# Kernel optimization log

Measured on AMD Instinct MI355X. Metric: run time of the kernel, lower is better.

Reference implementation:

```python
import jax, jax.numpy as jnp
import numpy as np

N_FILTERS = 40
FILTER_SIZE = 401   # int(16000*25/1000), forced odd
POOL_STRIDE = 160   # int(16000*10/1000)
EPS = 1e-6
S_SMOOTH = 0.04     # fixed PCEN smoothing coefficient s
DELTA = 2.0         # fixed PCEN bias delta
R_MIN, R_MAX = 0.2, 1.0
HIDDEN = 32


def setup_inputs() -> dict:
    key = jax.random.key(0)
    ks = jax.random.split(key, 6)
    B, L = 8, 160000
    x = jax.random.normal(ks[0], (B, L), dtype=jnp.float32)
    # mel-initialized Gabor params (as in mel_filter_params)
    sr, fmin, fmax = 16000.0, 60.0, 7800.0
    min_mel = 1127.0 * np.log1p(fmin / 700.0)
    max_mel = 1127.0 * np.log1p(fmax / 700.0)
    peaks_mel = np.linspace(min_mel, max_mel, N_FILTERS + 2)
    peaks_hz = 700.0 * np.expm1(peaks_mel / 1127.0)
    center_freqs = jnp.asarray(peaks_hz[1:-1] * 2.0 * np.pi / sr, dtype=jnp.float32)
    z = np.sqrt(2.0 * np.log(2.0)) / np.pi
    bandwidths = jnp.asarray(z * sr / (peaks_hz[2:] - peaks_hz[:-2]), dtype=jnp.float32)
    pooling_widths = jnp.full((N_FILTERS,), 0.4, dtype=jnp.float32)
    # GRU (input_size=1, hidden=32) + head Linear(32,32)->ReLU->Linear(32,2)
    def gl(k, shape):
        return jax.random.normal(k, shape, dtype=jnp.float32) * 0.1
    w_ih = gl(ks[1], (3 * HIDDEN, 1))
    w_hh = gl(ks[2], (3 * HIDDEN, HIDDEN))
    b_ih = jnp.zeros((3 * HIDDEN,), jnp.float32)
    b_hh = jnp.zeros((3 * HIDDEN,), jnp.float32)
    hw1 = gl(ks[3], (32, HIDDEN)); hb1 = jnp.zeros((32,), jnp.float32)
    hw2 = gl(ks[4], (2, 32)); hb2 = jnp.zeros((2,), jnp.float32)
    return dict(x=x, center_freqs=center_freqs, bandwidths=bandwidths,
                pooling_widths=pooling_widths, w_ih=w_ih, w_hh=w_hh,
                b_ih=b_ih, b_hh=b_hh, hw1=hw1, hb1=hb1, hw2=hw2, hb2=hb2)


def _gabor_filterbank(x, center_freqs, bandwidths, pooling_widths):
    z = np.sqrt(2.0 * np.log(2.0)) / np.pi
    cf = jnp.clip(center_freqs, 0.0, np.pi)
    bw = jnp.clip(bandwidths, 4.0 * z, FILTER_SIZE * z)
    t = jnp.arange(-(FILTER_SIZE // 2), (FILTER_SIZE + 1) // 2, dtype=jnp.float32)
    denom = 1.0 / (jnp.sqrt(2.0 * np.pi) * bw)                        # [F]
    gauss = jnp.exp(-(t[None, :] ** 2) / (2.0 * bw[:, None] ** 2))    # [F,K]
    phase = cf[:, None] * t[None, :]                                  # [F,K]
    fr = denom[:, None] * gauss * jnp.cos(phase)
    fi = denom[:, None] * gauss * jnp.sin(phase)
    filt = jnp.concatenate([fr, fi], axis=0)[:, None, :]              # [2F,1,K]
    pad = FILTER_SIZE // 2
    y = jax.lax.conv_general_dilated(x[:, None, :], filt, (1,), [(pad, pad)])
    y = y ** 2
    y = y[:, :N_FILTERS] + y[:, N_FILTERS:]                           # squared modulus [B,F,L]
    pw = jnp.clip(pooling_widths, 2.0 / FILTER_SIZE, 0.5)
    tt = jnp.arange(FILTER_SIZE, dtype=jnp.float32) / (FILTER_SIZE - 1) - 0.5
    win = jnp.exp(-0.5 * (tt[None, :] / pw[:, None]) ** 2)[:, None, :]  # [F,1,K]
    y = jax.lax.conv_general_dilated(y, win, (POOL_STRIDE,), [(pad, pad)],
                                     feature_group_count=N_FILTERS)
    return y  # [B,F,T]


def _gru_cell(h, xin, w_ih, w_hh, b_ih, b_hh):
    gi = xin @ w_ih.T + b_ih   # [N,3H]
    gh = h @ w_hh.T + b_hh
    i_r, i_z, i_n = jnp.split(gi, 3, axis=-1)
    h_r, h_z, h_n = jnp.split(gh, 3, axis=-1)
    r = jax.nn.sigmoid(i_r + h_r)
    zz = jax.nn.sigmoid(i_z + h_z)
    n = jnp.tanh(i_n + r * h_n)
    return (1.0 - zz) * n + zz * h


def _adaptive_pcen(frames, w_ih, w_hh, b_ih, b_hh, hw1, hb1, hw2, hb2):
    B, F, T = frames.shape
    Xt = jnp.transpose(frames, (2, 0, 1))  # [T,B,F]

    def controller(x_prev, x_t):  # each [B,F] -> per-bin (alpha, r)
        xp = x_prev.reshape(-1, 1)
        xc = x_t.reshape(-1, 1)
        h = jnp.zeros((B * F, HIDDEN), frames.dtype)
        h = _gru_cell(h, xp, w_ih, w_hh, b_ih, b_hh)
        h = _gru_cell(h, xc, w_ih, w_hh, b_ih, b_hh)
        hid = jax.nn.relu(h @ hw1.T + hb1)
        logits = hid @ hw2.T + hb2  # [B*F,2]
        alpha = jax.nn.sigmoid(logits[:, 0]).reshape(B, F)
        r = (R_MIN + (R_MAX - R_MIN) * jax.nn.sigmoid(logits[:, 1])).reshape(B, F)
        return alpha, r

    def step(carry, X_t):
        M_prev, X_prev = carry
        alpha, r = controller(X_prev, X_t)
        M_t = (1.0 - S_SMOOTH) * M_prev + S_SMOOTH * X_t
        out = (X_t / (M_t + EPS) ** alpha + DELTA) ** r - DELTA ** r
        return (M_t, X_t), out

    init = (jnp.zeros((B, F), frames.dtype), Xt[0])
    _, outs = jax.lax.scan(step, init, Xt)
    return jnp.transpose(outs, (1, 2, 0))  # [B,F,T]


def reference(x, center_freqs, bandwidths, pooling_widths,
              w_ih, w_hh, b_ih, b_hh, hw1, hb1, hw2, hb2):
    frames = _gabor_filterbank(x, center_freqs, bandwidths, pooling_widths)
    return _adaptive_pcen(frames, w_ih, w_hh, b_ih, b_hh, hw1, hb1, hw2, hb2)
```

## Files before the change

kernel.cpp:

```cpp
#include <hip/hip_runtime.h>
#include <math.h>

#define NF 40
#define FS 401
#define AST 424
#define PSTRIDE 160
#define BB 8
#define LL 160000
#define PADL 256
#define LST 161024
#define TOUT 1000
#define NTILE 512
#define NCHUNKC 313
#define ROWCH 121
#define ROWST (ROWCH*8)
#define EROW 520
#define TCP 32
#define NCHUNKP 32
#define PELEM (TCP*PSTRIDE + 408)
#define WROW 402
#define NCONVB 5032

typedef __attribute__((ext_vector_type(8))) _Float16 half8v;
typedef __attribute__((ext_vector_type(4))) _Float16 half4v;
typedef __attribute__((ext_vector_type(2))) _Float16 half2v;
typedef __attribute__((ext_vector_type(4))) float float4v;
typedef _Float16 f16;

__device__ __forceinline__ float sigm(float x) { return 1.0f / (1.0f + __expf(-x)); }
__device__ __forceinline__ float tanh_fast(float x) { return 1.0f - 2.0f / (__expf(2.0f * x) + 1.0f); }

__global__ __launch_bounds__(256) void prep_all(
    const float* __restrict__ x, const float* __restrict__ cf_,
    const float* __restrict__ bw_, const float* __restrict__ pw_,
    f16* __restrict__ xb, f16* __restrict__ Ag, float* __restrict__ winG)
{
    int blk = blockIdx.x;
    if (blk < NCONVB) {
        int i = blk * 256 + threadIdx.x;
        int b = i / LST, o = i % LST;
        float v = 0.0f;
        if (o >= PADL && o < PADL + LL) v = x[b * LL + (o - PADL)];
        xb[i] = (f16)v;
        return;
    }
    const float PI_F = 3.14159265358979323846f;
    if (blk < NCONVB + 80) {
        int row = blk - NCONVB;
        int f = row >> 1, comp = row & 1;
        float Z = sqrtf(2.0f * logf(2.0f)) / PI_F;
        float cf = fminf(fmaxf(cf_[f], 0.0f), PI_F);
        float bw = fminf(fmaxf(bw_[f], 4.0f * Z), 401.0f * Z);
        float denom = 1.0f / (sqrtf(2.0f * PI_F) * bw);
        float inv2 = 1.0f / (2.0f * bw * bw);
        for (int k = threadIdx.x; k < AST; k += 256) {
            float v = 0.0f;
            if (k < FS) {
                float t = (float)(k - 200);
                float g = denom * expf(-(t * t) * inv2);
                float sv, cv;
                sincosf(cf * t, &sv, &cv);
                v = comp ? g * sv : g * cv;
            }
            Ag[row * AST + k] = (f16)v;
        }
        return;
    }
    int f = blk - NCONVB - 80;
    float pw = fminf(fmaxf(pw_[f], 2.0f / 401.0f), 0.5f);
    float invpw = 1.0f / pw;
    for (int j = threadIdx.x; j < WROW; j += 256) {
        float w = 0.0f;
        if (j < FS) {
            float tt = (float)j * (1.0f / 400.0f) - 0.5f;
            float u = tt * invpw;
            w = expf(-0.5f * u * u);
        }
        winG[f * WROW + j] = w;
    }
}

__global__ __launch_bounds__(256, 2) void conv_mfma(
    const f16* __restrict__ xb,
    const f16* __restrict__ Ag,
    f16* __restrict__ eb)
{
    __shared__ __align__(16) unsigned char smem[40 * EROW * 2];
    f16* slab = (f16*)smem;
    f16* eL   = (f16*)smem;

    int chunk = blockIdx.x;
    int bi = blockIdx.y;
    int p0 = chunk * NTILE;
    int pbase = PADL + p0 - 200;
    const f16* xs = xb + (size_t)bi * LST;
    int tid = threadIdx.x;

    for (int sc = tid; sc < 8 * 120; sc += 256) {
        int r = sc / 120, m = sc - r * 120;
        int s0 = pbase + 8 * m + (r & ~1);
        const uint* gp = (const uint*)(xs + s0);
        uint v0 = gp[0], v1 = gp[1], v2 = gp[2], v3 = gp[3], v4 = gp[4];
        if (r & 1) {
            v0 = __builtin_amdgcn_alignbyte(v1, v0, 2);
            v1 = __builtin_amdgcn_alignbyte(v2, v1, 2);
            v2 = __builtin_amdgcn_alignbyte(v3, v2, 2);
            v3 = __builtin_amdgcn_alignbyte(v4, v3, 2);
        }
        *(uint4*)(&slab[r * ROWST + 8 * m]) = make_uint4(v0, v1, v2, v3);
    }
    __syncthreads();

    int wv = tid >> 6, lane = tid & 63, q = lane >> 4, l15 = lane & 15;

    float4v acc[5][8];
#pragma unroll
    for (int t = 0; t < 5; ++t)
#pragma unroll
        for (int s = 0; s < 8; ++s)
            acc[t][s] = (float4v){0.f, 0.f, 0.f, 0.f};

    const f16* aP[5];
    const f16* bPtr[10];
#pragma unroll
    for (int t = 0; t < 5; ++t) aP[t] = Ag + (16 * t + l15) * AST + 8 * q;
#pragma unroll
    for (int s = 0; s < 10; ++s) {
        int pos = 128 * wv + 16 * s + l15;
        bPtr[s] = slab + (pos & 7) * ROWST + 8 * ((pos >> 3) + q);
    }

    half8v bf[8];
#pragma unroll
    for (int s = 0; s < 8; ++s) bf[s] = *(const half8v*)(bPtr[s]);

#pragma unroll
    for (int kk = 0; kk < 13; ++kk) {
        int k = 32 * kk;
        half8v af[5];
#pragma unroll
        for (int t = 0; t < 5; ++t) af[t] = *(const half8v*)(aP[t] + k);
        half8v nb0, nb1;
        if (kk < 12) {
            nb0 = *(const half8v*)(bPtr[8] + k);
            nb1 = *(const half8v*)(bPtr[9] + k);
        }
#pragma unroll
        for (int t = 0; t < 5; ++t)
#pragma unroll
            for (int s = 0; s < 8; ++s)
                acc[t][s] = __builtin_amdgcn_mfma_f32_16x16x32_f16(af[t], bf[s], acc[t][s], 0, 0, 0);
        if (kk < 12) {
#pragma unroll
            for (int s = 0; s < 6; ++s) bf[s] = bf[s + 2];
            bf[6] = nb0; bf[7] = nb1;
        }
    }

    __syncthreads();

#pragma unroll
    for (int t = 0; t < 5; ++t) {
        int f0 = 8 * t + 2 * q;
#pragma unroll
        for (int s = 0; s < 8; ++s) {
            float4v a = acc[t][s];
            int pl = 128 * wv + 16 * s + l15;
            eL[f0 * EROW + pl] = (f16)(a.x * a.x + a.y * a.y);
            eL[(f0 + 1) * EROW + pl] = (f16)(a.z * a.z + a.w * a.w);
        }
    }
    __syncthreads();

    f16* ebb = eb + (size_t)bi * NF * LL;
#pragma unroll
    for (int it = 0; it < 10; ++it) {
        int idx = it * 256 + tid;
        int row = idx >> 6;
        int off = (idx & 63) * 8;
        if (p0 + off < LL) {
            uint4 v = *(const uint4*)(&eL[row * EROW + off]);
            *(uint4*)(&ebb[row * LL + p0 + off]) = v;
        }
    }
}

__global__ __launch_bounds__(256) void pool_kernel(
    const f16* __restrict__ eb, const float* __restrict__ winG, float* __restrict__ Xout)
{
    __shared__ __align__(16) f16 es[PELEM + 8];
    __shared__ __align__(16) float win[416];
    int chunk = blockIdx.x;
    int f = blockIdx.y;
    int bi = blockIdx.z;
    int tau0 = chunk * TCP;
    int start = tau0 * PSTRIDE - 200;
    int tid = threadIdx.x;

    for (int k = tid; k < 416; k += 256)
        win[k] = (k < WROW) ? winG[f * WROW + k] : 0.0f;

    const f16* erow = eb + ((size_t)bi * NF + f) * LL;
    if (start >= 0 && start + PELEM <= LL) {
        for (int j = tid; j < PELEM / 8; j += 256)
            *(uint4*)(&es[8 * j]) = *(const uint4*)(erow + start + 8 * j);
    } else {
        for (int j = tid; j < PELEM; j += 256) {
            int p = start + j;
            es[j] = (p >= 0 && p < LL) ? erow[p] : (f16)0.0f;
        }
    }
    __syncthreads();

    int ft = tid >> 4, l16 = tid & 15;
#pragma unroll
    for (int pass = 0; pass < 2; ++pass) {
        int frame = pass * 16 + ft;
        int base = frame * PSTRIDE;
        float acc = 0.0f;
#pragma unroll
        for (int m = 0; m < 13; ++m) {
            int kw = 2 * l16 + 32 * m;
            half2v ep = *(const half2v*)(&es[base + kw]);
            float2 wp = *(const float2*)(&win[kw]);
            acc = fmaf((float)ep[0], wp.x, acc);
            acc = fmaf((float)ep[1], wp.y, acc);
        }
#pragma unroll
        for (int off = 8; off > 0; off >>= 1)
            acc += __shfl_down(acc, off, 16);
        int tau = tau0 + frame;
        if (l16 == 0 && tau < TOUT)
            Xout[((size_t)bi * NF + f) * TOUT + tau] = acc;
    }
}

__global__ __launch_bounds__(256) void pcen_scan_kernel(
    const float* __restrict__ X, float* __restrict__ M)
{
    int wid = (blockIdx.x * 256 + threadIdx.x) >> 6;
    int lane = threadIdx.x & 63;
    if (wid >= BB * NF) return;
    const float a1 = 0.96f;
    const float a2 = a1 * a1;
    const float a4 = a2 * a2;
    const float a8 = a4 * a4;
    const float a16 = a8 * a8;
    const float a32 = a16 * a16;
    const float ss = 0.04f;
    float al1 = powf(a1, (float)(lane + 1));
    float carry = 0.0f;
    const float* row = X + wid * TOUT;
    float* mrow = M + wid * TOUT;

    for (int c = 0; c < TOUT; c += 64) {
        int t = c + lane;
        float v = (t < TOUT) ? row[t] : 0.0f;
        float y = ss * v;
        float u;
        u = __shfl_up(y, 1, 64);  if (lane >= 1)  y = fmaf(a1, u, y);
        u = __shfl_up(y, 2, 64);  if (lane >= 2)  y = fmaf(a2, u, y);
        u = __shfl_up(y, 4, 64);  if (lane >= 4)  y = fmaf(a4, u, y);
        u = __shfl_up(y, 8, 64);  if (lane >= 8)  y = fmaf(a8, u, y);
        u = __shfl_up(y, 16, 64); if (lane >= 16) y = fmaf(a16, u, y);
        u = __shfl_up(y, 32, 64); if (lane >= 32) y = fmaf(a32, u, y);
        y = fmaf(al1, carry, y);
        carry = __shfl(y, 63, 64);
        if (t < TOUT) mrow[t] = y;
    }
}

__global__ __launch_bounds__(256) void pcen_ctrl_mfma(
    const float* __restrict__ X, const float* __restrict__ M,
    const float* __restrict__ w_ih, const float* __restrict__ w_hh,
    const float* __restrict__ b_ih, const float* __restrict__ b_hh,
    const float* __restrict__ hw1, const float* __restrict__ hb1,
    const float* __restrict__ hw2, const float* __restrict__ hb2,
    float* __restrict__ out)
{
    __shared__ f16 s_whhA[96 * 40];
    __shared__ f16 s_w1A[32 * 40];
    __shared__ __align__(16) float4 s_A1[32];
    __shared__ __align__(16) float4 s_A2[32];
    __shared__ float s_hb1[32];
    __shared__ float s_hw2[64];
    __shared__ float s_hb2[2];
    __shared__ f16 sh1[4][16 * 40];
    __shared__ f16 sh2[4][16 * 40];

    int tid = threadIdx.x;
    for (int i = tid; i < 96 * 32; i += 256) {
        int m = i >> 5, k = i & 31;
        s_whhA[m * 40 + k] = (f16)w_hh[i];
    }
    for (int i = tid; i < 32 * 32; i += 256) {
        int m = i >> 5, k = i & 31;
        s_w1A[m * 40 + k] = (f16)hw1[i];
    }
    if (tid < 32) {
        int j = tid;
        s_A1[j] = make_float4(w_ih[j], b_ih[j] + b_hh[j],
                              w_ih[32 + j], b_ih[32 + j] + b_hh[32 + j]);
        s_A2[j] = make_float4(w_ih[64 + j], b_ih[64 + j], b_hh[64 + j], 0.0f);
        s_hb1[j] = hb1[j];
    }
    if (tid < 64) s_hw2[tid] = hw2[tid];
    if (tid < 2)  s_hb2[tid] = hb2[tid];
    __syncthreads();

    int wv = tid >> 6, lane = tid & 63;
    int c = lane & 15, q = lane >> 4;
    int waveBase = blockIdx.x * 256 + wv * 64;

#pragma unroll
    for (int g = 0; g < 4; ++g) {
        int idx0 = waveBase + g * 16;
        int idxc = idx0 + c;
        int tt0 = idx0 % TOUT + c;
        float xc = X[idxc];
        float xp = (tt0 == 0 || tt0 == TOUT) ? xc : X[idxc - 1];
        float mv = M[idxc];

        float h1v[8];
#pragma unroll
        for (int jj = 0; jj < 8; ++jj) {
            int j = (jj < 4) ? (4 * q + jj) : (16 + 4 * q + (jj - 4));
            float4 a1 = s_A1[j];
            float4 a2 = s_A2[j];
            float r = sigm(fmaf(xp, a1.x, a1.y));
            float z = sigm(fmaf(xp, a1.z, a1.w));
            float n = tanh_fast(fmaf(xp, a2.x, a2.y) + r * a2.z);
            h1v[jj] = (1.0f - z) * n;
        }

        {
            half4v lo = {(f16)h1v[0], (f16)h1v[1], (f16)h1v[2], (f16)h1v[3]};
            half4v hi = {(f16)h1v[4], (f16)h1v[5], (f16)h1v[6], (f16)h1v[7]};
            *(half4v*)(&sh1[wv][c * 40 + 4 * q]) = lo;
            *(half4v*)(&sh1[wv][c * 40 + 16 + 4 * q]) = hi;
        }

        float4v acc[6];
        {
            half8v bfv = *(const half8v*)(&sh1[wv][c * 40 + 8 * q]);
#pragma unroll
            for (int t = 0; t < 6; ++t) {
                half8v af = *(const half8v*)(&s_whhA[(16 * t + c) * 40 + 8 * q]);
                acc[t] = __builtin_amdgcn_mfma_f32_16x16x32_f16(af, bfv, (float4v){0.f,0.f,0.f,0.f}, 0, 0, 0);
            }
        }

        float h2v[8];
#pragma unroll
        for (int jj = 0; jj < 8; ++jj) {
            int j = (jj < 4) ? (4 * q + jj) : (16 + 4 * q + (jj - 4));
            int reg = jj & 3;
            float accR = (jj < 4) ? acc[0][reg] : acc[1][reg];
            float accZ = (jj < 4) ? acc[2][reg] : acc[3][reg];
            float accN = (jj < 4) ? acc[4][reg] : acc[5][reg];
            float4 a1 = s_A1[j];
            float4 a2 = s_A2[j];
            float r = sigm(fmaf(xc, a1.x, a1.y) + accR);
            float z = sigm(fmaf(xc, a1.z, a1.w) + accZ);
            float gn = accN + a2.z;
            float n = tanh_fast(fmaf(xc, a2.x, a2.y) + r * gn);
            h2v[jj] = fmaf(z, h1v[jj] - n, n);
        }

        {
            half4v lo = {(f16)h2v[0], (f16)h2v[1], (f16)h2v[2], (f16)h2v[3]};
            half4v hi = {(f16)h2v[4], (f16)h2v[5], (f16)h2v[6], (f16)h2v[7]};
            *(half4v*)(&sh2[wv][c * 40 + 4 * q]) = lo;
            *(half4v*)(&sh2[wv][c * 40 + 16 + 4 * q]) = hi;
        }

        float4v hacc[2];
        {
            half8v bfv = *(const half8v*)(&sh2[wv][c * 40 + 8 * q]);
#pragma unroll
            for (int t = 0; t < 2; ++t) {
                half8v af = *(const half8v*)(&s_w1A[(16 * t + c) * 40 + 8 * q]);
                hacc[t] = __builtin_amdgcn_mfma_f32_16x16x32_f16(af, bfv, (float4v){0.f,0.f,0.f,0.f}, 0, 0, 0);
            }
        }

        float p0 = 0.f, p1 = 0.f;
#pragma unroll
        for (int jj = 0; jj < 8; ++jj) {
            int i = (jj < 4) ? (4 * q + jj) : (16 + 4 * q + (jj - 4));
            int reg = jj & 3;
            float hv = (jj < 4) ? hacc[0][reg] : hacc[1][reg];
            hv = fmaxf(hv + s_hb1[i], 0.0f);
            p0 = fmaf(hv, s_hw2[i], p0);
            p1 = fmaf(hv, s_hw2[32 + i], p1);
        }
        p0 += __shfl_xor(p0, 16);
        p0 += __shfl_xor(p0, 32);
        p1 += __shfl_xor(p1, 16);
        p1 += __shfl_xor(p1, 32);

        float alpha = sigm(p0 + s_hb2[0]);
        float rr = fmaf(0.8f, sigm(p1 + s_hb2[1]), 0.2f);
        float md = __expf(alpha * __logf(mv + 1e-6f));
        float bse = xc / md + 2.0f;
        float val = __expf(rr * __logf(bse)) - __expf(rr * 0.69314718056f);
        if (q == 0)
            out[idxc] = val;
    }
}

extern "C" void kernel_launch(void* const* d_in, const int* in_sizes, int n_in,
                              void* d_out, int out_size, void* d_ws, size_t ws_size,
                              hipStream_t stream) {
    const float* x    = (const float*)d_in[0];
    const float* cf   = (const float*)d_in[1];
    const float* bw   = (const float*)d_in[2];
    const float* pw   = (const float*)d_in[3];
    const float* w_ih = (const float*)d_in[4];
    const float* w_hh = (const float*)d_in[5];
    const float* b_ih = (const float*)d_in[6];
    const float* b_hh = (const float*)d_in[7];
    const float* hw1  = (const float*)d_in[8];
    const float* hb1  = (const float*)d_in[9];
    const float* hw2  = (const float*)d_in[10];
    const float* hb2  = (const float*)d_in[11];
    float* out = (float*)d_out;

    const size_t xb_b = (size_t)BB * LST * 2;
    const size_t ag_b = (size_t)80 * AST * 2;
    const size_t wg_b = (size_t)NF * WROW * 4;
    const size_t xm_b = (size_t)2 * BB * NF * TOUT * 4;
    size_t fixed = xb_b + ag_b + wg_b + xm_b;
    size_t e_per_batch = (size_t)NF * LL * 2;
    int nb;
    if (ws_size >= fixed + 8 * e_per_batch)      nb = 8;
    else if (ws_size >= fixed + 2 * e_per_batch) nb = 2;
    else                                         nb = 1;
    int nslice = BB / nb;

    f16* xb    = (f16*)d_ws;
    f16* Ag    = xb + (size_t)BB * LST;
    float* winG = (float*)(Ag + (size_t)80 * AST);
    f16* ebuf  = (f16*)(winG + (size_t)NF * WROW);
    float* Xf  = (float*)(ebuf + (size_t)nb * NF * LL);
    float* Mf  = Xf + (size_t)BB * NF * TOUT;

    prep_all<<<dim3(NCONVB + 80 + NF), dim3(256), 0, stream>>>(x, cf, bw, pw, xb, Ag, winG);

    for (int sl = 0; sl < nslice; ++sl) {
        conv_mfma<<<dim3(NCHUNKC, nb), dim3(256), 0, stream>>>(
            xb + (size_t)sl * nb * LST, Ag, ebuf);
        pool_kernel<<<dim3(NCHUNKP, NF, nb), dim3(256), 0, stream>>>(
            ebuf, winG, Xf + (size_t)sl * nb * NF * TOUT);
    }

    pcen_scan_kernel<<<dim3((BB * NF * 64) / 256), dim3(256), 0, stream>>>(Xf, Mf);
    pcen_ctrl_mfma<<<dim3((BB * NF * TOUT) / 256), dim3(256), 0, stream>>>(
        Xf, Mf, w_ih, w_hh, b_ih, b_hh, hw1, hb1, hw2, hb2, out);
}
```

Measured before the change: 265.9 us.

## Fuse pooling, PCEN scan and controller into one per-row tail kernel

Replaces the pool, scan and controller kernels with a single 1024-thread block per (batch, filter) row. The block pools the row in eight shared-memory chunks, runs the smoothing scan in shared memory, then evaluates the GRU controller and PCEN output. This removes two launches and the global round trips for the X and M intermediates. In exchange the tail runs on only 40×nb blocks with a serial chunk loop and a single-wave scan, so GPU occupancy and parallelism drop sharply.

```diff
diff --git a/kernel.cpp b/kernel.cpp
--- a/kernel.cpp
+++ b/kernel.cpp
@@ -15,11 +15,10 @@
 #define ROWCH 121
 #define ROWST (ROWCH*8)
 #define EROW 520
-#define TCP 32
-#define NCHUNKP 32
-#define PELEM (TCP*PSTRIDE + 408)
 #define WROW 402
 #define NCONVB 5032
+#define TAUC 125
+#define ECH (TAUC*PSTRIDE + 408)
 
 typedef __attribute__((ext_vector_type(8))) _Float16 half8v;
 typedef __attribute__((ext_vector_type(4))) _Float16 half4v;
@@ -185,99 +184,18 @@
     }
 }
 
-__global__ __launch_bounds__(256) void pool_kernel(
-    const f16* __restrict__ eb, const float* __restrict__ winG, float* __restrict__ Xout)
-{
-    __shared__ __align__(16) f16 es[PELEM + 8];
-    __shared__ __align__(16) float win[416];
-    int chunk = blockIdx.x;
-    int f = blockIdx.y;
-    int bi = blockIdx.z;
-    int tau0 = chunk * TCP;
-    int start = tau0 * PSTRIDE - 200;
-    int tid = threadIdx.x;
-
-    for (int k = tid; k < 416; k += 256)
-        win[k] = (k < WROW) ? winG[f * WROW + k] : 0.0f;
-
-    const f16* erow = eb + ((size_t)bi * NF + f) * LL;
-    if (start >= 0 && start + PELEM <= LL) {
-        for (int j = tid; j < PELEM / 8; j += 256)
-            *(uint4*)(&es[8 * j]) = *(const uint4*)(erow + start + 8 * j);
-    } else {
-        for (int j = tid; j < PELEM; j += 256) {
-            int p = start + j;
-            es[j] = (p >= 0 && p < LL) ? erow[p] : (f16)0.0f;
-        }
-    }
-    __syncthreads();
-
-    int ft = tid >> 4, l16 = tid & 15;
-#pragma unroll
-    for (int pass = 0; pass < 2; ++pass) {
-        int frame = pass * 16 + ft;
-        int base = frame * PSTRIDE;
-        float acc = 0.0f;
-#pragma unroll
-        for (int m = 0; m < 13; ++m) {
-            int kw = 2 * l16 + 32 * m;
-            half2v ep = *(const half2v*)(&es[base + kw]);
-            float2 wp = *(const float2*)(&win[kw]);
-            acc = fmaf((float)ep[0], wp.x, acc);
-            acc = fmaf((float)ep[1], wp.y, acc);
-        }
-#pragma unroll
-        for (int off = 8; off > 0; off >>= 1)
-            acc += __shfl_down(acc, off, 16);
-        int tau = tau0 + frame;
-        if (l16 == 0 && tau < TOUT)
-            Xout[((size_t)bi * NF + f) * TOUT + tau] = acc;
-    }
-}
-
-__global__ __launch_bounds__(256) void pcen_scan_kernel(
-    const float* __restrict__ X, float* __restrict__ M)
-{
-    int wid = (blockIdx.x * 256 + threadIdx.x) >> 6;
-    int lane = threadIdx.x & 63;
-    if (wid >= BB * NF) return;
-    const float a1 = 0.96f;
-    const float a2 = a1 * a1;
-    const float a4 = a2 * a2;
-    const float a8 = a4 * a4;
-    const float a16 = a8 * a8;
-    const float a32 = a16 * a16;
-    const float ss = 0.04f;
-    float al1 = powf(a1, (float)(lane + 1));
-    float carry = 0.0f;
-    const float* row = X + wid * TOUT;
-    float* mrow = M + wid * TOUT;
-
-    for (int c = 0; c < TOUT; c += 64) {
-        int t = c + lane;
-        float v = (t < TOUT) ? row[t] : 0.0f;
-        float y = ss * v;
-        float u;
-        u = __shfl_up(y, 1, 64);  if (lane >= 1)  y = fmaf(a1, u, y);
-        u = __shfl_up(y, 2, 64);  if (lane >= 2)  y = fmaf(a2, u, y);
-        u = __shfl_up(y, 4, 64);  if (lane >= 4)  y = fmaf(a4, u, y);
-        u = __shfl_up(y, 8, 64);  if (lane >= 8)  y = fmaf(a8, u, y);
-        u = __shfl_up(y, 16, 64); if (lane >= 16) y = fmaf(a16, u, y);
-        u = __shfl_up(y, 32, 64); if (lane >= 32) y = fmaf(a32, u, y);
-        y = fmaf(al1, carry, y);
-        carry = __shfl(y, 63, 64);
-        if (t < TOUT) mrow[t] = y;
-    }
-}
-
-__global__ __launch_bounds__(256) void pcen_ctrl_mfma(
-    const float* __restrict__ X, const float* __restrict__ M,
+__global__ __launch_bounds__(1024, 4) void tail_kernel(
+    const f16* __restrict__ eb,
+    const float* __restrict__ winG,
     const float* __restrict__ w_ih, const float* __restrict__ w_hh,
     const float* __restrict__ b_ih, const float* __restrict__ b_hh,
     const float* __restrict__ hw1, const float* __restrict__ hb1,
     const float* __restrict__ hw2, const float* __restrict__ hb2,
     float* __restrict__ out)
 {
+    __shared__ __align__(16) float win[416];
+    __shared__ __align__(16) float xs[1024];
+    __shared__ __align__(16) float ms[1024];
     __shared__ f16 s_whhA[96 * 40];
     __shared__ f16 s_w1A[32 * 40];
     __shared__ __align__(16) float4 s_A1[32];
@@ -285,15 +203,18 @@
     __shared__ float s_hb1[32];
     __shared__ float s_hw2[64];
     __shared__ float s_hb2[2];
-    __shared__ f16 sh1[4][16 * 40];
-    __shared__ f16 sh2[4][16 * 40];
-
+    __shared__ __align__(16) unsigned char ureg[41024];
+    f16* es = (f16*)ureg;
+
+    int f = blockIdx.x;
+    int bi = blockIdx.y;
     int tid = threadIdx.x;
-    for (int i = tid; i < 96 * 32; i += 256) {
+
+    for (int i = tid; i < 96 * 32; i += 1024) {
         int m = i >> 5, k = i & 31;
         s_whhA[m * 40 + k] = (f16)w_hh[i];
     }
-    for (int i = tid; i < 32 * 32; i += 256) {
+    for (int i = tid; i < 32 * 32; i += 1024) {
         int m = i >> 5, k = i & 31;
         s_w1A[m * 40 + k] = (f16)hw1[i];
     }
@@ -306,20 +227,83 @@
     }
     if (tid < 64) s_hw2[tid] = hw2[tid];
     if (tid < 2)  s_hb2[tid] = hb2[tid];
+    if (tid < 416) win[tid] = (tid < WROW) ? winG[f * WROW + tid] : 0.0f;
+    if (tid >= 1000) { xs[tid] = 0.0f; ms[tid] = 0.0f; }
     __syncthreads();
 
+    const f16* erow = eb + ((size_t)bi * NF + f) * LL;
+    int ft = tid >> 4, l16 = tid & 15;
+    for (int c = 0; c < 8; ++c) {
+        int start = c * (TAUC * PSTRIDE) - 200;
+        if (c > 0 && c < 7) {
+            for (int j = tid; j < ECH / 8; j += 1024)
+                *(uint4*)(&es[8 * j]) = *(const uint4*)(erow + start + 8 * j);
+        } else {
+            for (int j = tid; j < ECH; j += 1024) {
+                int p = start + j;
+                es[j] = (p >= 0 && p < LL) ? erow[p] : (f16)0.0f;
+            }
+        }
+        __syncthreads();
+#pragma unroll
+        for (int pass = 0; pass < 2; ++pass) {
+            int tauL = pass * 64 + ft;
+            if (tauL < TAUC) {
+                int base = tauL * PSTRIDE;
+                float acc = 0.0f;
+#pragma unroll
+                for (int m = 0; m < 13; ++m) {
+                    int kw = 2 * l16 + 32 * m;
+                    half2v ep = *(const half2v*)(&es[base + kw]);
+                    float2 wp = *(const float2*)(&win[kw]);
+                    acc = fmaf((float)ep[0], wp.x, acc);
+                    acc = fmaf((float)ep[1], wp.y, acc);
+                }
+#pragma unroll
+                for (int off = 8; off > 0; off >>= 1)
+                    acc += __shfl_down(acc, off, 16);
+                if (l16 == 0) xs[c * TAUC + tauL] = acc;
+            }
+        }
+        __syncthreads();
+    }
+
+    if (tid < 64) {
+        int lane = tid;
+        const float a1 = 0.96f;
+        const float a2 = a1 * a1, a4 = a2 * a2, a8 = a4 * a4;
+        const float a16 = a8 * a8, a32 = a16 * a16;
+        float al1 = powf(a1, (float)(lane + 1));
+        float carry = 0.0f;
+        for (int c = 0; c < TOUT; c += 64) {
+            float y = 0.04f * xs[c + lane];
+            float u;
+            u = __shfl_up(y, 1, 64);  if (lane >= 1)  y = fmaf(a1, u, y);
+            u = __shfl_up(y, 2, 64);  if (lane >= 2)  y = fmaf(a2, u, y);
+            u = __shfl_up(y, 4, 64);  if (lane >= 4)  y = fmaf(a4, u, y);
+            u = __shfl_up(y, 8, 64);  if (lane >= 8)  y = fmaf(a8, u, y);
+            u = __shfl_up(y, 16, 64); if (lane >= 16) y = fmaf(a16, u, y);
+            u = __shfl_up(y, 32, 64); if (lane >= 32) y = fmaf(a32, u, y);
+            y = fmaf(al1, carry, y);
+            carry = __shfl(y, 63, 64);
+            ms[c + lane] = y;
+        }
+    }
+    __syncthreads();
+
     int wv = tid >> 6, lane = tid & 63;
-    int c = lane & 15, q = lane >> 4;
-    int waveBase = blockIdx.x * 256 + wv * 64;
+    int c16 = lane & 15, q = lane >> 4;
+    f16* sh1 = (f16*)(ureg + wv * 2560);
+    f16* sh2 = (f16*)(ureg + wv * 2560 + 1280);
+    float* outb = out + ((size_t)bi * NF + f) * TOUT;
 
 #pragma unroll
     for (int g = 0; g < 4; ++g) {
-        int idx0 = waveBase + g * 16;
-        int idxc = idx0 + c;
-        int tt0 = idx0 % TOUT + c;
-        float xc = X[idxc];
-        float xp = (tt0 == 0 || tt0 == TOUT) ? xc : X[idxc - 1];
-        float mv = M[idxc];
+        int t = (wv * 4 + g) * 16 + c16;
+        int tc = (t < TOUT) ? t : (TOUT - 1);
+        float xc = xs[tc];
+        float xp = (tc == 0) ? xc : xs[tc - 1];
+        float mv = ms[tc];
 
         float h1v[8];
 #pragma unroll
@@ -332,24 +316,21 @@
             float n = tanh_fast(fmaf(xp, a2.x, a2.y) + r * a2.z);
             h1v[jj] = (1.0f - z) * n;
         }
-
         {
             half4v lo = {(f16)h1v[0], (f16)h1v[1], (f16)h1v[2], (f16)h1v[3]};
             half4v hi = {(f16)h1v[4], (f16)h1v[5], (f16)h1v[6], (f16)h1v[7]};
-            *(half4v*)(&sh1[wv][c * 40 + 4 * q]) = lo;
-            *(half4v*)(&sh1[wv][c * 40 + 16 + 4 * q]) = hi;
-        }
-
+            *(half4v*)(&sh1[c16 * 40 + 4 * q]) = lo;
+            *(half4v*)(&sh1[c16 * 40 + 16 + 4 * q]) = hi;
+        }
         float4v acc[6];
         {
-            half8v bfv = *(const half8v*)(&sh1[wv][c * 40 + 8 * q]);
-#pragma unroll
-            for (int t = 0; t < 6; ++t) {
-                half8v af = *(const half8v*)(&s_whhA[(16 * t + c) * 40 + 8 * q]);
-                acc[t] = __builtin_amdgcn_mfma_f32_16x16x32_f16(af, bfv, (float4v){0.f,0.f,0.f,0.f}, 0, 0, 0);
+            half8v bfv = *(const half8v*)(&sh1[c16 * 40 + 8 * q]);
+#pragma unroll
+            for (int tt = 0; tt < 6; ++tt) {
+                half8v af = *(const half8v*)(&s_whhA[(16 * tt + c16) * 40 + 8 * q]);
+                acc[tt] = __builtin_amdgcn_mfma_f32_16x16x32_f16(af, bfv, (float4v){0.f,0.f,0.f,0.f}, 0, 0, 0);
             }
         }
-
         float h2v[8];
 #pragma unroll
         for (int jj = 0; jj < 8; ++jj) {
@@ -366,24 +347,21 @@
             float n = tanh_fast(fmaf(xc, a2.x, a2.y) + r * gn);
             h2v[jj] = fmaf(z, h1v[jj] - n, n);
         }
-
         {
             half4v lo = {(f16)h2v[0], (f16)h2v[1], (f16)h2v[2], (f16)h2v[3]};
             half4v hi = {(f16)h2v[4], (f16)h2v[5], (f16)h2v[6], (f16)h2v[7]};
-            *(half4v*)(&sh2[wv][c * 40 + 4 * q]) = lo;
-            *(half4v*)(&sh2[wv][c * 40 + 16 + 4 * q]) = hi;
-        }
-
+            *(half4v*)(&sh2[c16 * 40 + 4 * q]) = lo;
+            *(half4v*)(&sh2[c16 * 40 + 16 + 4 * q]) = hi;
+        }
         float4v hacc[2];
         {
-            half8v bfv = *(const half8v*)(&sh2[wv][c * 40 + 8 * q]);
-#pragma unroll
-            for (int t = 0; t < 2; ++t) {
-                half8v af = *(const half8v*)(&s_w1A[(16 * t + c) * 40 + 8 * q]);
-                hacc[t] = __builtin_amdgcn_mfma_f32_16x16x32_f16(af, bfv, (float4v){0.f,0.f,0.f,0.f}, 0, 0, 0);
+            half8v bfv = *(const half8v*)(&sh2[c16 * 40 + 8 * q]);
+#pragma unroll
+            for (int tt = 0; tt < 2; ++tt) {
+                half8v af = *(const half8v*)(&s_w1A[(16 * tt + c16) * 40 + 8 * q]);
+                hacc[tt] = __builtin_amdgcn_mfma_f32_16x16x32_f16(af, bfv, (float4v){0.f,0.f,0.f,0.f}, 0, 0, 0);
             }
         }
-
         float p0 = 0.f, p1 = 0.f;
 #pragma unroll
         for (int jj = 0; jj < 8; ++jj) {
@@ -404,8 +382,8 @@
         float md = __expf(alpha * __logf(mv + 1e-6f));
         float bse = xc / md + 2.0f;
         float val = __expf(rr * __logf(bse)) - __expf(rr * 0.69314718056f);
-        if (q == 0)
-            out[idxc] = val;
+        if (q == 0 && t < TOUT)
+            outb[t] = val;
     }
 }
 
@@ -429,8 +407,7 @@
     const size_t xb_b = (size_t)BB * LST * 2;
     const size_t ag_b = (size_t)80 * AST * 2;
     const size_t wg_b = (size_t)NF * WROW * 4;
-    const size_t xm_b = (size_t)2 * BB * NF * TOUT * 4;
-    size_t fixed = xb_b + ag_b + wg_b + xm_b;
+    size_t fixed = xb_b + ag_b + wg_b;
     size_t e_per_batch = (size_t)NF * LL * 2;
     int nb;
     if (ws_size >= fixed + 8 * e_per_batch)      nb = 8;
@@ -438,23 +415,18 @@
     else                                         nb = 1;
     int nslice = BB / nb;
 
-    f16* xb    = (f16*)d_ws;
-    f16* Ag    = xb + (size_t)BB * LST;
+    f16* xb     = (f16*)d_ws;
+    f16* Ag     = xb + (size_t)BB * LST;
     float* winG = (float*)(Ag + (size_t)80 * AST);
-    f16* ebuf  = (f16*)(winG + (size_t)NF * WROW);
-    float* Xf  = (float*)(ebuf + (size_t)nb * NF * LL);
-    float* Mf  = Xf + (size_t)BB * NF * TOUT;
+    f16* ebuf   = (f16*)(winG + (size_t)NF * WROW);
 
     prep_all<<<dim3(NCONVB + 80 + NF), dim3(256), 0, stream>>>(x, cf, bw, pw, xb, Ag, winG);
 
     for (int sl = 0; sl < nslice; ++sl) {
         conv_mfma<<<dim3(NCHUNKC, nb), dim3(256), 0, stream>>>(
             xb + (size_t)sl * nb * LST, Ag, ebuf);
-        pool_kernel<<<dim3(NCHUNKP, NF, nb), dim3(256), 0, stream>>>(
-            ebuf, winG, Xf + (size_t)sl * nb * NF * TOUT);
-    }
-
-    pcen_scan_kernel<<<dim3((BB * NF * 64) / 256), dim3(256), 0, stream>>>(Xf, Mf);
-    pcen_ctrl_mfma<<<dim3((BB * NF * TOUT) / 256), dim3(256), 0, stream>>>(
-        Xf, Mf, w_ih, w_hh, b_ih, b_hh, hw1, hb1, hw2, hb2, out);
+        tail_kernel<<<dim3(NF, nb), dim3(1024), 0, stream>>>(
+            ebuf, winG, w_ih, w_hh, b_ih, b_hh, hw1, hb1, hw2, hb2,
+            out + (size_t)sl * nb * NF * TOUT);
+    }
 }
```

New measurement: 299.6 us. +12.7%, slower.

## Shrink conv LDS staging via two-pass epilogue; spread PCEN controller over more blocks

Applied to the files above, without the earlier changes.

The conv epilogue now writes the squared-magnitude tile to LDS in two passes (16 filters, then 24), so the shared buffer shrinks from 40 rows to 24. That lowers LDS use per block and may allow more resident blocks, at the cost of extra barriers. The PCEN controller kernel now has each wave handle 16 outputs instead of looping over 64, launching four times as many blocks to raise parallelism. The cost is repeated per-block weight staging into LDS.

```diff
diff --git a/kernel.cpp b/kernel.cpp
--- a/kernel.cpp
+++ b/kernel.cpp
@@ -15,10 +15,10 @@
 #define ROWCH 121
 #define ROWST (ROWCH*8)
 #define EROW 520
+#define WROW 402
 #define TCP 32
 #define NCHUNKP 32
 #define PELEM (TCP*PSTRIDE + 408)
-#define WROW 402
 #define NCONVB 5032
 
 typedef __attribute__((ext_vector_type(8))) _Float16 half8v;
@@ -85,7 +85,7 @@
     const f16* __restrict__ Ag,
     f16* __restrict__ eb)
 {
-    __shared__ __align__(16) unsigned char smem[40 * EROW * 2];
+    __shared__ __align__(16) unsigned char smem[24 * EROW * 2];
     f16* slab = (f16*)smem;
     f16* eL   = (f16*)smem;
 
@@ -159,8 +159,10 @@
 
     __syncthreads();
 
-#pragma unroll
-    for (int t = 0; t < 5; ++t) {
+    f16* ebb = eb + (size_t)bi * NF * LL;
+
+#pragma unroll
+    for (int t = 0; t < 2; ++t) {
         int f0 = 8 * t + 2 * q;
 #pragma unroll
         for (int s = 0; s < 8; ++s) {
@@ -171,16 +173,38 @@
         }
     }
     __syncthreads();
-
-    f16* ebb = eb + (size_t)bi * NF * LL;
-#pragma unroll
-    for (int it = 0; it < 10; ++it) {
+#pragma unroll
+    for (int it = 0; it < 4; ++it) {
         int idx = it * 256 + tid;
         int row = idx >> 6;
         int off = (idx & 63) * 8;
         if (p0 + off < LL) {
             uint4 v = *(const uint4*)(&eL[row * EROW + off]);
             *(uint4*)(&ebb[row * LL + p0 + off]) = v;
+        }
+    }
+    __syncthreads();
+
+#pragma unroll
+    for (int t = 2; t < 5; ++t) {
+        int f0 = 8 * t + 2 * q;
+#pragma unroll
+        for (int s = 0; s < 8; ++s) {
+            float4v a = acc[t][s];
+            int pl = 128 * wv + 16 * s + l15;
+            eL[(f0 - 16) * EROW + pl] = (f16)(a.x * a.x + a.y * a.y);
+            eL[(f0 - 15) * EROW + pl] = (f16)(a.z * a.z + a.w * a.w);
+        }
+    }
+    __syncthreads();
+#pragma unroll
+    for (int it = 0; it < 6; ++it) {
+        int idx = it * 256 + tid;
+        int row = idx >> 6;
+        int off = (idx & 63) * 8;
+        if (p0 + off < LL) {
+            uint4 v = *(const uint4*)(&eL[row * EROW + off]);
+            *(uint4*)(&ebb[(row + 16) * LL + p0 + off]) = v;
         }
     }
 }
@@ -310,103 +334,99 @@
 
     int wv = tid >> 6, lane = tid & 63;
     int c = lane & 15, q = lane >> 4;
-    int waveBase = blockIdx.x * 256 + wv * 64;
-
-#pragma unroll
-    for (int g = 0; g < 4; ++g) {
-        int idx0 = waveBase + g * 16;
-        int idxc = idx0 + c;
-        int tt0 = idx0 % TOUT + c;
-        float xc = X[idxc];
-        float xp = (tt0 == 0 || tt0 == TOUT) ? xc : X[idxc - 1];
-        float mv = M[idxc];
-
-        float h1v[8];
-#pragma unroll
-        for (int jj = 0; jj < 8; ++jj) {
-            int j = (jj < 4) ? (4 * q + jj) : (16 + 4 * q + (jj - 4));
-            float4 a1 = s_A1[j];
-            float4 a2 = s_A2[j];
-            float r = sigm(fmaf(xp, a1.x, a1.y));
-            float z = sigm(fmaf(xp, a1.z, a1.w));
-            float n = tanh_fast(fmaf(xp, a2.x, a2.y) + r * a2.z);
-            h1v[jj] = (1.0f - z) * n;
-        }
-
-        {
-            half4v lo = {(f16)h1v[0], (f16)h1v[1], (f16)h1v[2], (f16)h1v[3]};
-            half4v hi = {(f16)h1v[4], (f16)h1v[5], (f16)h1v[6], (f16)h1v[7]};
-            *(half4v*)(&sh1[wv][c * 40 + 4 * q]) = lo;
-            *(half4v*)(&sh1[wv][c * 40 + 16 + 4 * q]) = hi;
-        }
-
-        float4v acc[6];
-        {
-            half8v bfv = *(const half8v*)(&sh1[wv][c * 40 + 8 * q]);
-#pragma unroll
-            for (int t = 0; t < 6; ++t) {
-                half8v af = *(const half8v*)(&s_whhA[(16 * t + c) * 40 + 8 * q]);
-                acc[t] = __builtin_amdgcn_mfma_f32_16x16x32_f16(af, bfv, (float4v){0.f,0.f,0.f,0.f}, 0, 0, 0);
-            }
-        }
-
-        float h2v[8];
-#pragma unroll
-        for (int jj = 0; jj < 8; ++jj) {
-            int j = (jj < 4) ? (4 * q + jj) : (16 + 4 * q + (jj - 4));
-            int reg = jj & 3;
-            float accR = (jj < 4) ? acc[0][reg] : acc[1][reg];
-            float accZ = (jj < 4) ? acc[2][reg] : acc[3][reg];
-            float accN = (jj < 4) ? acc[4][reg] : acc[5][reg];
-            float4 a1 = s_A1[j];
-            float4 a2 = s_A2[j];
-            float r = sigm(fmaf(xc, a1.x, a1.y) + accR);
-            float z = sigm(fmaf(xc, a1.z, a1.w) + accZ);
-            float gn = accN + a2.z;
-            float n = tanh_fast(fmaf(xc, a2.x, a2.y) + r * gn);
-            h2v[jj] = fmaf(z, h1v[jj] - n, n);
-        }
-
-        {
-            half4v lo = {(f16)h2v[0], (f16)h2v[1], (f16)h2v[2], (f16)h2v[3]};
-            half4v hi = {(f16)h2v[4], (f16)h2v[5], (f16)h2v[6], (f16)h2v[7]};
-            *(half4v*)(&sh2[wv][c * 40 + 4 * q]) = lo;
-            *(half4v*)(&sh2[wv][c * 40 + 16 + 4 * q]) = hi;
-        }
-
-        float4v hacc[2];
-        {
-            half8v bfv = *(const half8v*)(&sh2[wv][c * 40 + 8 * q]);
-#pragma unroll
-            for (int t = 0; t < 2; ++t) {
-                half8v af = *(const half8v*)(&s_w1A[(16 * t + c) * 40 + 8 * q]);
-                hacc[t] = __builtin_amdgcn_mfma_f32_16x16x32_f16(af, bfv, (float4v){0.f,0.f,0.f,0.f}, 0, 0, 0);
-            }
-        }
-
-        float p0 = 0.f, p1 = 0.f;
-#pragma unroll
-        for (int jj = 0; jj < 8; ++jj) {
-            int i = (jj < 4) ? (4 * q + jj) : (16 + 4 * q + (jj - 4));
-            int reg = jj & 3;
-            float hv = (jj < 4) ? hacc[0][reg] : hacc[1][reg];
-            hv = fmaxf(hv + s_hb1[i], 0.0f);
-            p0 = fmaf(hv, s_hw2[i], p0);
-            p1 = fmaf(hv, s_hw2[32 + i], p1);
-        }
-        p0 += __shfl_xor(p0, 16);
-        p0 += __shfl_xor(p0, 32);
-        p1 += __shfl_xor(p1, 16);
-        p1 += __shfl_xor(p1, 32);
-
-        float alpha = sigm(p0 + s_hb2[0]);
-        float rr = fmaf(0.8f, sigm(p1 + s_hb2[1]), 0.2f);
-        float md = __expf(alpha * __logf(mv + 1e-6f));
-        float bse = xc / md + 2.0f;
-        float val = __expf(rr * __logf(bse)) - __expf(rr * 0.69314718056f);
-        if (q == 0)
-            out[idxc] = val;
-    }
+    int instBase = blockIdx.x * 64 + wv * 16;
+
+    int idx = instBase + c;
+    int t = idx % TOUT;
+    float xc = X[idx];
+    float xp = (t == 0) ? xc : X[idx - 1];
+    float mv = M[idx];
+
+    float h1v[8];
+#pragma unroll
+    for (int jj = 0; jj < 8; ++jj) {
+        int j = (jj < 4) ? (4 * q + jj) : (16 + 4 * q + (jj - 4));
+        float4 a1 = s_A1[j];
+        float4 a2 = s_A2[j];
+        float r = sigm(fmaf(xp, a1.x, a1.y));
+        float z = sigm(fmaf(xp, a1.z, a1.w));
+        float n = tanh_fast(fmaf(xp, a2.x, a2.y) + r * a2.z);
+        h1v[jj] = (1.0f - z) * n;
+    }
+
+    {
+        half4v lo = {(f16)h1v[0], (f16)h1v[1], (f16)h1v[2], (f16)h1v[3]};
+        half4v hi = {(f16)h1v[4], (f16)h1v[5], (f16)h1v[6], (f16)h1v[7]};
+        *(half4v*)(&sh1[wv][c * 40 + 4 * q]) = lo;
+        *(half4v*)(&sh1[wv][c * 40 + 16 + 4 * q]) = hi;
+    }
+
+    float4v acc[6];
+    {
+        half8v bf = *(const half8v*)(&sh1[wv][c * 40 + 8 * q]);
+#pragma unroll
+        for (int tt = 0; tt < 6; ++tt) {
+            half8v af = *(const half8v*)(&s_whhA[(16 * tt + c) * 40 + 8 * q]);
+            acc[tt] = __builtin_amdgcn_mfma_f32_16x16x32_f16(af, bf, (float4v){0.f,0.f,0.f,0.f}, 0, 0, 0);
+        }
+    }
+
+    float h2v[8];
+#pragma unroll
+    for (int jj = 0; jj < 8; ++jj) {
+        int j = (jj < 4) ? (4 * q + jj) : (16 + 4 * q + (jj - 4));
+        int reg = jj & 3;
+        float accR = (jj < 4) ? acc[0][reg] : acc[1][reg];
+        float accZ = (jj < 4) ? acc[2][reg] : acc[3][reg];
+        float accN = (jj < 4) ? acc[4][reg] : acc[5][reg];
+        float4 a1 = s_A1[j];
+        float4 a2 = s_A2[j];
+        float r = sigm(fmaf(xc, a1.x, a1.y) + accR);
+        float z = sigm(fmaf(xc, a1.z, a1.w) + accZ);
+        float gn = accN + a2.z;
+        float n = tanh_fast(fmaf(xc, a2.x, a2.y) + r * gn);
+        h2v[jj] = fmaf(z, h1v[jj] - n, n);
+    }
+
+    {
+        half4v lo = {(f16)h2v[0], (f16)h2v[1], (f16)h2v[2], (f16)h2v[3]};
+        half4v hi = {(f16)h2v[4], (f16)h2v[5], (f16)h2v[6], (f16)h2v[7]};
+        *(half4v*)(&sh2[wv][c * 40 + 4 * q]) = lo;
+        *(half4v*)(&sh2[wv][c * 40 + 16 + 4 * q]) = hi;
+    }
+
+    float4v hacc[2];
+    {
+        half8v bf = *(const half8v*)(&sh2[wv][c * 40 + 8 * q]);
+#pragma unroll
+        for (int tt = 0; tt < 2; ++tt) {
+            half8v af = *(const half8v*)(&s_w1A[(16 * tt + c) * 40 + 8 * q]);
+            hacc[tt] = __builtin_amdgcn_mfma_f32_16x16x32_f16(af, bf, (float4v){0.f,0.f,0.f,0.f}, 0, 0, 0);
+        }
+    }
+
+    float p0 = 0.f, p1 = 0.f;
+#pragma unroll
+    for (int jj = 0; jj < 8; ++jj) {
+        int i = (jj < 4) ? (4 * q + jj) : (16 + 4 * q + (jj - 4));
+        int reg = jj & 3;
+        float hv = (jj < 4) ? hacc[0][reg] : hacc[1][reg];
+        hv = fmaxf(hv + s_hb1[i], 0.0f);
+        p0 = fmaf(hv, s_hw2[i], p0);
+        p1 = fmaf(hv, s_hw2[32 + i], p1);
+    }
+    p0 += __shfl_xor(p0, 16);
+    p0 += __shfl_xor(p0, 32);
+    p1 += __shfl_xor(p1, 16);
+    p1 += __shfl_xor(p1, 32);
+
+    float alpha = sigm(p0 + s_hb2[0]);
+    float rr = fmaf(0.8f, sigm(p1 + s_hb2[1]), 0.2f);
+    float md = __expf(alpha * __logf(mv + 1e-6f));
+    float bse = xc / md + 2.0f;
+    float val = __expf(rr * __logf(bse)) - __expf(rr * 0.69314718056f);
+    if (lane < 16)
+        out[idx] = val;
 }
 
 extern "C" void kernel_launch(void* const* d_in, const int* in_sizes, int n_in,
@@ -438,12 +458,12 @@
     else                                         nb = 1;
     int nslice = BB / nb;
 
-    f16* xb    = (f16*)d_ws;
-    f16* Ag    = xb + (size_t)BB * LST;
+    f16* xb     = (f16*)d_ws;
+    f16* Ag     = xb + (size_t)BB * LST;
     float* winG = (float*)(Ag + (size_t)80 * AST);
-    f16* ebuf  = (f16*)(winG + (size_t)NF * WROW);
-    float* Xf  = (float*)(ebuf + (size_t)nb * NF * LL);
-    float* Mf  = Xf + (size_t)BB * NF * TOUT;
+    f16* ebuf   = (f16*)(winG + (size_t)NF * WROW);
+    float* Xf   = (float*)(ebuf + (size_t)nb * NF * LL);
+    float* Mf   = Xf + (size_t)BB * NF * TOUT;
 
     prep_all<<<dim3(NCONVB + 80 + NF), dim3(256), 0, stream>>>(x, cf, bw, pw, xb, Ag, winG);
 
@@ -455,6 +475,6 @@
     }
 
     pcen_scan_kernel<<<dim3((BB * NF * 64) / 256), dim3(256), 0, stream>>>(Xf, Mf);
-    pcen_ctrl_mfma<<<dim3((BB * NF * TOUT) / 256), dim3(256), 0, stream>>>(
+    pcen_ctrl_mfma<<<dim3((BB * NF * TOUT) / 64), dim3(256), 0, stream>>>(
         Xf, Mf, w_ih, w_hh, b_ih, b_hh, hw1, hb1, hw2, hb2, out);
 }
```

New measurement: 263.3 us. No clear change (-1.0%).
